# Kernel optimization log

Measured on AMD Instinct MI355X. Metric: run time of the kernel, lower is better.

## Reference

```python
import jax, jax.numpy as jnp
import numpy as np
import math

D_MODEL = 1024
FEAT = 16            # feature_dim
HEADS = 16
HEAD_DIM = D_MODEL // HEADS          # 64
EXP = 1 + FEAT + FEAT * FEAT         # 273, expanded (Taylor) feature dim
BATCH = 4
SEQ = 2048


def taylor_exp(x):
    """2nd-order Taylor feature map: [1, x/d^{1/4}, (x ox x)/(sqrt(2)*sqrt(d))]."""
    d = x.shape[-1]
    r2 = math.sqrt(2.0)
    rd = math.sqrt(d)
    rrd = math.sqrt(rd)
    x2 = (x[..., :, None] * x[..., None, :]).reshape(*x.shape[:-1], d * d) / r2
    return jnp.concatenate([jnp.ones_like(x[..., :1]), x / rrd, x2 / rd], axis=-1)


def setup_inputs() -> dict:
    key = jax.random.key(0)
    ks = jax.random.split(key, 9)
    s_in = 1.0 / math.sqrt(D_MODEL)
    inp = {
        "x": jax.random.normal(ks[0], (BATCH, SEQ, D_MODEL), dtype=jnp.float32),
        "kv_state": jnp.zeros((BATCH, HEADS, EXP, HEAD_DIM), dtype=jnp.float32),
        "k_state": jnp.zeros((BATCH, HEADS, EXP), dtype=jnp.float32),
        # Linear params stored as [in, out] (y = x @ W + b)
        "Wq": jax.random.normal(ks[1], (D_MODEL, FEAT * HEADS), dtype=jnp.float32) * s_in,
        "bq": jnp.zeros((FEAT * HEADS,), dtype=jnp.float32),
        "Wk": jax.random.normal(ks[2], (D_MODEL, FEAT * HEADS), dtype=jnp.float32) * s_in,
        "bk": jnp.zeros((FEAT * HEADS,), dtype=jnp.float32),
        "Wv": jax.random.normal(ks[3], (D_MODEL, HEAD_DIM * HEADS), dtype=jnp.float32) * s_in,
        "bv": jnp.zeros((HEAD_DIM * HEADS,), dtype=jnp.float32),
        "Wo": jax.random.normal(ks[4], (HEADS * HEAD_DIM, D_MODEL), dtype=jnp.float32) * s_in,
        "bo": jnp.zeros((D_MODEL,), dtype=jnp.float32),
    }
    return inp


def _forward(x, kv_state, k_state, Wq, bq, Wk, bk, Wv, bv, Wo, bo):
    b, l, _ = x.shape
    # projections -> b h l d
    q = (x @ Wq + bq).reshape(b, l, HEADS, FEAT).transpose(0, 2, 1, 3)
    k = (x @ Wk + bk).reshape(b, l, HEADS, FEAT).transpose(0, 2, 1, 3)
    v = (x @ Wv + bv).reshape(b, l, HEADS, HEAD_DIM).transpose(0, 2, 1, 3)
    q = taylor_exp(q)  # b h l EXP
    k = taylor_exp(k)  # b h l EXP

    # scan over time: carry (kv_state [b,h,EXP,hd], k_state [b,h,EXP])
    qs = jnp.moveaxis(q, 2, 0)  # l b h EXP
    ks = jnp.moveaxis(k, 2, 0)  # l b h EXP
    vs = jnp.moveaxis(v, 2, 0)  # l b h hd

    def step(carry, qkv_t):
        kv, kst = carry
        q_t, k_t, v_t = qkv_t
        kv = kv + k_t[..., :, None] * v_t[..., None, :]   # b h EXP hd
        kst = kst + k_t                                    # b h EXP
        num = jnp.einsum('bhd,bhdc->bhc', q_t, kv)
        den = jnp.einsum('bhd,bhd->bh', q_t, kst) + 1e-6
        return (kv, kst), num / den[..., None]

    (kv_f, kst_f), outs = jax.lax.scan(step, (kv_state, k_state), (qs, ks, vs))
    # outs: l b h hd -> b l (h hd)
    y = jnp.moveaxis(outs, 0, 1).reshape(b, l, HEADS * HEAD_DIM)
    y = y @ Wo + bo  # dropout is identity in eval mode
    return y, kv_f, kst_f


def reference(x, kv_state, k_state, Wq, bq, Wk, bk, Wv, bv, Wo, bo):
    return _forward(x, kv_state, k_state, Wq, bq, Wk, bk, Wv, bv, Wo, bo)
```

## Files before the change

### kernel.cpp

```cpp
#include <hip/hip_runtime.h>

typedef unsigned short u16;
typedef __attribute__((ext_vector_type(8))) short bf16x8;
typedef __attribute__((ext_vector_type(4))) float f32x4;

#define BATCH 4
#define SEQ   2048
#define DM    1024
#define HEADS 16
#define FEAT  16
#define HD    64
#define EXPD  273
#define EXPP  288
#define CHK   128
#define NC    16
#define BH    64
#define QKS   512
#define MROWS 8192
#define C2    0.17677669529663687f

__device__ __forceinline__ u16 f2b(float f) {
  union { float f; unsigned u; } v; v.f = f;
  unsigned u = v.u;
  return (u16)((u + 0x7fffu + ((u >> 16) & 1u)) >> 16);
}
__device__ __forceinline__ float b2f(u16 s) {
  union { unsigned u; float f; } v; v.u = ((unsigned)s) << 16; return v.f;
}

typedef const unsigned int __attribute__((address_space(1)))* gas1;
typedef unsigned int __attribute__((address_space(3)))* las3;
__device__ __forceinline__ void gl_lds16(const u16* g, u16* l) {
  __builtin_amdgcn_global_load_lds((gas1)(const void*)g, (las3)(void*)l, 16, 0, 0);
}

__global__ __launch_bounds__(256) void prep(const float* __restrict__ x, u16* __restrict__ xb,
                                            const float* __restrict__ Wq, const float* __restrict__ Wk,
                                            const float* __restrict__ Wv, const float* __restrict__ Wo,
                                            u16* __restrict__ wqkvT, u16* __restrict__ woT,
                                            const float* __restrict__ bq, const float* __restrict__ bk,
                                            const float* __restrict__ bv, float* __restrict__ bias_all) {
  __shared__ float tile[32][33];
  int id = blockIdx.x;
  if (id < 8192) {
    int i = id * 256 + threadIdx.x;
    float4 v = ((const float4*)x)[i];
    u16 r[4] = {f2b(v.x), f2b(v.y), f2b(v.z), f2b(v.w)};
    ((uint2*)xb)[i] = *(uint2*)r;
    return;
  }
  id -= 8192;
  if (id < 2560) {
    const float* src; u16* dst; int N, t;
    if (id < 256)       { src = Wq; dst = wqkvT;            N = 256;  t = id; }
    else if (id < 512)  { src = Wk; dst = wqkvT + 256 * DM; N = 256;  t = id - 256; }
    else if (id < 1536) { src = Wv; dst = wqkvT + 512 * DM; N = 1024; t = id - 512; }
    else                { src = Wo; dst = woT;              N = 1024; t = id - 1536; }
    int nt = N / 32;
    int n0 = (t % nt) * 32, k0 = (t / nt) * 32;
    int tx = threadIdx.x & 31, ty = threadIdx.x >> 5;
    for (int i = ty; i < 32; i += 8)
      tile[i][tx] = src[(size_t)(k0 + i) * N + n0 + tx];
    __syncthreads();
    for (int i = ty; i < 32; i += 8)
      dst[(size_t)(n0 + i) * DM + k0 + tx] = f2b(tile[tx][i]);
    return;
  }
  id -= 2560;
  int i = id * 256 + threadIdx.x;
  float v;
  if (i < 256) v = bq[i];
  else if (i < 512) v = bk[i - 256];
  else v = bv[i - 512];
  bias_all[i] = v;
}

__global__ __launch_bounds__(256) void gemmQKV(const u16* __restrict__ A, const u16* __restrict__ BT,
                                               const float* __restrict__ bias,
                                               float* __restrict__ qkw, u16* __restrict__ vbT) {
  __shared__ __align__(16) u16 As[128 * 32];
  __shared__ __align__(16) u16 Bs[128 * 32];
  const int tid = threadIdx.x;
  const int wave = tid >> 6, lane = tid & 63, qd = lane >> 4, ln = lane & 15;
  const int wr = (wave >> 1) * 64, wc = (wave & 1) * 64;
  const int m0 = blockIdx.y * 128, n0 = blockIdx.x * 128;
  const int K = DM;
  f32x4 acc[4][4];
#pragma unroll
  for (int i = 0; i < 4; i++)
#pragma unroll
    for (int j = 0; j < 4; j++) acc[i][j] = (f32x4){0.f, 0.f, 0.f, 0.f};
  const int sr = tid >> 2, sk = (tid & 3) * 8;
  const u16* gA0 = A + (size_t)(m0 + sr) * K + sk;
  const u16* gA1 = A + (size_t)(m0 + 64 + sr) * K + sk;
  const u16* gB0 = BT + (size_t)(n0 + sr) * K + sk;
  const u16* gB1 = BT + (size_t)(n0 + 64 + sr) * K + sk;
  u16* lA0 = &As[(size_t)(wave * 64) * 8];
  u16* lA1 = &As[(size_t)(256 + wave * 64) * 8];
  u16* lB0 = &Bs[(size_t)(wave * 64) * 8];
  u16* lB1 = &Bs[(size_t)(256 + wave * 64) * 8];
  for (int kk = 0; kk < K; kk += 32) {
    gl_lds16(gA0 + kk, lA0);
    gl_lds16(gA1 + kk, lA1);
    gl_lds16(gB0 + kk, lB0);
    gl_lds16(gB1 + kk, lB1);
    __syncthreads();
    bf16x8 af[4], bf[4];
#pragma unroll
    for (int t = 0; t < 4; t++) {
      af[t] = *(const bf16x8*)&As[(wr + t * 16 + ln) * 32 + qd * 8];
      bf[t] = *(const bf16x8*)&Bs[(wc + t * 16 + ln) * 32 + qd * 8];
    }
#pragma unroll
    for (int mt = 0; mt < 4; mt++)
#pragma unroll
      for (int nt = 0; nt < 4; nt++)
        acc[mt][nt] = __builtin_amdgcn_mfma_f32_16x16x32_bf16(af[mt], bf[nt], acc[mt][nt], 0, 0, 0);
    __syncthreads();
  }
  if (n0 < 512) {
#pragma unroll
    for (int nt = 0; nt < 4; nt++) {
      int col = n0 + wc + nt * 16 + ln;
      float bv = bias[col];
#pragma unroll
      for (int mt = 0; mt < 4; mt++)
#pragma unroll
        for (int r = 0; r < 4; r++) {
          int row = m0 + wr + mt * 16 + qd * 4 + r;
          qkw[(size_t)row * QKS + col] = acc[mt][nt][r] + bv;
        }
    }
  } else {
#pragma unroll
    for (int nt = 0; nt < 4; nt++) {
      int col = n0 + wc + nt * 16 + ln;
      float bv = bias[col];
      int vcol = col - 512;
#pragma unroll
      for (int mt = 0; mt < 4; mt++) {
        u16 pk[4];
#pragma unroll
        for (int r = 0; r < 4; r++) pk[r] = f2b(acc[mt][nt][r] + bv);
        int row0 = m0 + wr + mt * 16 + qd * 4;
        *(uint2*)&vbT[(size_t)vcol * MROWS + row0] = *(uint2*)pk;
      }
    }
  }
}

__global__ __launch_bounds__(256) void gemm128(const u16* __restrict__ A, const u16* __restrict__ BT,
                                               const float* __restrict__ bias, int M, int N, int K,
                                               float* __restrict__ outF) {
  __shared__ __align__(16) u16 As[128 * 32];
  __shared__ __align__(16) u16 Bs[128 * 32];
  const int tid = threadIdx.x;
  const int wave = tid >> 6, lane = tid & 63, qd = lane >> 4, ln = lane & 15;
  const int wr = (wave >> 1) * 64, wc = (wave & 1) * 64;
  const int m0 = blockIdx.y * 128, n0 = blockIdx.x * 128;
  f32x4 acc[4][4];
#pragma unroll
  for (int i = 0; i < 4; i++)
#pragma unroll
    for (int j = 0; j < 4; j++) acc[i][j] = (f32x4){0.f, 0.f, 0.f, 0.f};
  const int sr = tid >> 2, sk = (tid & 3) * 8;
  const u16* gA0 = A + (size_t)(m0 + sr) * K + sk;
  const u16* gA1 = A + (size_t)(m0 + 64 + sr) * K + sk;
  const u16* gB0 = BT + (size_t)(n0 + sr) * K + sk;
  const u16* gB1 = BT + (size_t)(n0 + 64 + sr) * K + sk;
  u16* lA0 = &As[(size_t)(wave * 64) * 8];
  u16* lA1 = &As[(size_t)(256 + wave * 64) * 8];
  u16* lB0 = &Bs[(size_t)(wave * 64) * 8];
  u16* lB1 = &Bs[(size_t)(256 + wave * 64) * 8];
  for (int kk = 0; kk < K; kk += 32) {
    gl_lds16(gA0 + kk, lA0);
    gl_lds16(gA1 + kk, lA1);
    gl_lds16(gB0 + kk, lB0);
    gl_lds16(gB1 + kk, lB1);
    __syncthreads();
    bf16x8 af[4], bf[4];
#pragma unroll
    for (int t = 0; t < 4; t++) {
      af[t] = *(const bf16x8*)&As[(wr + t * 16 + ln) * 32 + qd * 8];
      bf[t] = *(const bf16x8*)&Bs[(wc + t * 16 + ln) * 32 + qd * 8];
    }
#pragma unroll
    for (int mt = 0; mt < 4; mt++)
#pragma unroll
      for (int nt = 0; nt < 4; nt++)
        acc[mt][nt] = __builtin_amdgcn_mfma_f32_16x16x32_bf16(af[mt], bf[nt], acc[mt][nt], 0, 0, 0);
    __syncthreads();
  }
#pragma unroll
  for (int nt = 0; nt < 4; nt++) {
    int col = n0 + wc + nt * 16 + ln;
    float bv = bias[col];
#pragma unroll
    for (int mt = 0; mt < 4; mt++)
#pragma unroll
      for (int r = 0; r < 4; r++) {
        int row = m0 + wr + mt * 16 + qd * 4 + r;
        outF[(size_t)row * N + col] = acc[mt][nt][r] + bv;
      }
  }
}

template<int KT>
__device__ __forceinline__ void feat_row(const float* q16, int p, u16* dst) {
  u16 pk[16];
  if (KT == 0 && p == 0) {
    pk[0] = 0x3F80;
#pragma unroll
    for (int j = 1; j < 16; j++) pk[j] = f2b(0.5f * q16[j - 1]);
  } else if (KT == 0) {
    pk[0] = f2b(0.5f * q16[15]);
    float wm = C2 * q16[0];
#pragma unroll
    for (int j = 1; j < 16; j++) pk[j] = f2b(wm * q16[j - 1]);
  } else {
    constexpr int c = 2 * KT;
    float wm = C2 * (p ? q16[c]     : q16[c - 1]);
    float w0 = C2 * (p ? q16[c - 1] : q16[c - 2]);
    pk[0] = f2b(w0 * q16[15]);
#pragma unroll
    for (int j = 1; j < 16; j++) pk[j] = f2b(wm * q16[j - 1]);
    if (KT == 8 && p) {
#pragma unroll
      for (int j = 1; j < 16; j++) pk[j] = 0;
    }
  }
  *(uint4*)dst = *(uint4*)pk;
  *(uint4*)(dst + 8) = *(uint4*)(pk + 8);
}

template<int MTB>
__device__ __forceinline__ void kfeat(const float* k16, int p, int t2, u16 (*kfT)[16][136]) {
  u16 pk[16];
  if (MTB == 0) {
    if (p == 0) {
      pk[0] = 0x3F80;
#pragma unroll
      for (int j = 1; j < 16; j++) pk[j] = f2b(0.5f * k16[j - 1]);
    } else {
      float w0 = C2 * k16[0], wm = C2 * k16[1];
      pk[0] = f2b(w0 * k16[15]);
#pragma unroll
      for (int j = 1; j < 16; j++) pk[j] = f2b(wm * k16[j - 1]);
    }
  } else if (MTB == 1) {
    if (p == 0) {
      pk[0] = f2b(0.5f * k16[15]);
      float wm = C2 * k16[0];
#pragma unroll
      for (int j = 1; j < 16; j++) pk[j] = f2b(wm * k16[j - 1]);
    } else {
      float w0 = C2 * k16[1], wm = C2 * k16[2];
      pk[0] = f2b(w0 * k16[15]);
#pragma unroll
      for (int j = 1; j < 16; j++) pk[j] = f2b(wm * k16[j - 1]);
    }
  } else {
    float wm = C2 * (p ? k16[MTB + 1] : k16[MTB - 1]);
    float w0 = C2 * (p ? k16[MTB]     : k16[MTB - 2]);
    pk[0] = f2b(w0 * k16[15]);
#pragma unroll
    for (int j = 1; j < 16; j++) pk[j] = f2b(wm * k16[j - 1]);
  }
  int b = 2 * p + (MTB & 1);
#pragma unroll
  for (int el = 0; el < 16; el++) kfT[b][el][t2] = pk[el];
}

__global__ __launch_bounds__(256) void chunk_sums(const float* __restrict__ qkw, const u16* __restrict__ vbT,
                                                  u16* __restrict__ ckvT, float* __restrict__ ck) {
  __shared__ float kl[CHK][20];
  __shared__ __align__(16) u16 kfT[4][16][136];
  const int tid = threadIdx.x;
  const int bh = blockIdx.x / NC, c = blockIdx.x % NC;
  const int b = bh >> 4, h = bh & 15;
  const int wave = tid >> 6, lane = tid & 63, qd = lane >> 4, ln = lane & 15;
  const int t2 = tid >> 1, p = tid & 1;
  const size_t rowbase = (size_t)(b * SEQ + c * CHK);
  float k16[16];
  {
    const float* kp = &qkw[(rowbase + t2) * QKS + 256 + h * FEAT];
    float4 v0 = *(const float4*)kp, v1 = *(const float4*)(kp + 4);
    float4 v2 = *(const float4*)(kp + 8), v3 = *(const float4*)(kp + 12);
    k16[0] = v0.x; k16[1] = v0.y; k16[2] = v0.z; k16[3] = v0.w;
    k16[4] = v1.x; k16[5] = v1.y; k16[6] = v1.z; k16[7] = v1.w;
    k16[8] = v2.x; k16[9] = v2.y; k16[10] = v2.z; k16[11] = v2.w;
    k16[12] = v3.x; k16[13] = v3.y; k16[14] = v3.z; k16[15] = v3.w;
    float4 h0, h1;
    if (p == 0) { h0 = v0; h1 = v1; } else { h0 = v2; h1 = v3; }
    *(float4*)&kl[t2][p * 8] = h0;
    *(float4*)&kl[t2][p * 8 + 4] = h1;
  }
  uint4 bVv[4][4];
#pragma unroll
  for (int kk2 = 0; kk2 < 4; kk2++)
#pragma unroll
    for (int nt = 0; nt < 4; nt++)
      bVv[kk2][nt] = *(const uint4*)&vbT[(size_t)(h * HD + nt * 16 + ln) * MROWS +
                                         rowbase + kk2 * 32 + qd * 8];
  const size_t obase = (size_t)(bh * NC + c) * HD;
  auto mstore = [&](int mt, int bufw) {
    f32x4 acc[4];
#pragma unroll
    for (int nt = 0; nt < 4; nt++) acc[nt] = (f32x4){0.f, 0.f, 0.f, 0.f};
#pragma unroll
    for (int kk2 = 0; kk2 < 4; kk2++) {
      bf16x8 a = *(const bf16x8*)&kfT[bufw][ln][kk2 * 32 + qd * 8];
#pragma unroll
      for (int nt = 0; nt < 4; nt++) {
        bf16x8 bb = *(const bf16x8*)&bVv[kk2][nt];
        acc[nt] = __builtin_amdgcn_mfma_f32_16x16x32_bf16(a, bb, acc[nt], 0, 0, 0);
      }
    }
#pragma unroll
    for (int nt = 0; nt < 4; nt++) {
      u16 pk[4];
#pragma unroll
      for (int r = 0; r < 4; r++) pk[r] = f2b(acc[nt][r]);
      *(uint2*)&ckvT[(obase + nt * 16 + ln) * EXPP + mt * 16 + qd * 4] = *(uint2*)pk;
    }
  };
  __syncthreads();
  kfeat<0>(k16, p, t2, kfT); kfeat<1>(k16, p, t2, kfT);
  __syncthreads();
  mstore(wave, wave);
  __syncthreads();
  kfeat<4>(k16, p, t2, kfT); kfeat<5>(k16, p, t2, kfT);
  __syncthreads();
  mstore(4 + wave, wave);
  __syncthreads();
  kfeat<8>(k16, p, t2, kfT); kfeat<9>(k16, p, t2, kfT);
  __syncthreads();
  mstore(8 + wave, wave);
  __syncthreads();
  kfeat<12>(k16, p, t2, kfT); kfeat<13>(k16, p, t2, kfT);
  __syncthreads();
  mstore(12 + wave, wave);
  __syncthreads();
  {
    u16 pk[16];
    if (p == 0) {
      float w0 = C2 * k16[14], wm = C2 * k16[15];
      pk[0] = f2b(w0 * k16[15]);
#pragma unroll
      for (int j = 1; j < 16; j++) pk[j] = f2b(wm * k16[j - 1]);
    } else {
      pk[0] = f2b(C2 * k16[15] * k16[15]);
#pragma unroll
      for (int j = 1; j < 16; j++) pk[j] = 0;
    }
#pragma unroll
    for (int el = 0; el < 16; el++) kfT[p][el][t2] = pk[el];
  }
  __syncthreads();
  if (wave < 2) mstore(16 + wave, wave);
  for (int e = tid; e < EXPP; e += 256) {
    float s = 0.f;
    if (e == 0) s = (float)CHK;
    else if (e < 17) { float t = 0.f; for (int tt = 0; tt < CHK; tt++) t += kl[tt][e - 1]; s = 0.5f * t; }
    else if (e < EXPD) {
      int u = e - 17, i0 = u >> 4, j0 = u & 15; float t = 0.f;
      for (int tt = 0; tt < CHK; tt++) t += kl[tt][i0] * kl[tt][j0];
      s = C2 * t;
    }
    ck[(size_t)(bh * NC + c) * EXPP + e] = s;
  }
}

__global__ __launch_bounds__(256) void kv_prefix(u16* __restrict__ ckvT, const float* __restrict__ kv0,
                                                 float* __restrict__ out_kv,
                                                 float* __restrict__ ck, const float* __restrict__ k0,
                                                 float* __restrict__ out_k) {
  const int tid = threadIdx.x;
  const int bh = blockIdx.x / 10, eg = blockIdx.x % 10;
  if (eg == 9) {
    for (int e = tid; e < EXPP; e += 256) {
      float S = (e < EXPD) ? k0[(size_t)bh * EXPD + e] : 0.f;
      for (int c = 0; c < NC; c++) {
        size_t idx = ((size_t)bh * NC + c) * EXPP + e;
        float v = ck[idx];
        ck[idx] = S;
        S += v;
      }
      if (e < EXPD) out_k[(size_t)bh * EXPD + e] = S;
    }
    return;
  }
  const int hd = tid >> 2;
  const int e0 = eg * 32 + (tid & 3) * 8;
  float S[8];
#pragma unroll
  for (int j = 0; j < 8; j++) {
    int e = e0 + j;
    S[j] = (e < EXPD) ? kv0[((size_t)bh * EXPD + e) * HD + hd] : 0.f;
  }
  u16* base = ckvT + ((size_t)bh * NC * HD + hd) * EXPP + e0;
  const size_t cstride = (size_t)HD * EXPP;
  uint4 v0 = *(const uint4*)base;
  uint4 v1 = *(const uint4*)(base + cstride);
  for (int c = 0; c < NC; c++) {
    uint4 vn = v1;
    if (c + 2 < NC) vn = *(const uint4*)(base + (size_t)(c + 2) * cstride);
    union { uint4 q; u16 s[8]; } pk;
#pragma unroll
    for (int j = 0; j < 8; j++) pk.s[j] = f2b(S[j]);
    *(uint4*)(base + (size_t)c * cstride) = pk.q;
    union { uint4 q; u16 s[8]; } vv; vv.q = v0;
#pragma unroll
    for (int j = 0; j < 8; j++) S[j] += b2f(vv.s[j]);
    v0 = v1; v1 = vn;
  }
#pragma unroll
  for (int j = 0; j < 8; j++) {
    int e = e0 + j;
    if (e < EXPD) out_kv[((size_t)bh * EXPD + e) * HD + hd] = S[j];
  }
}

__global__ __launch_bounds__(256) void out_chunk(const float* __restrict__ qkw, const u16* __restrict__ vbT,
                                                 const u16* __restrict__ ckvT, const float* __restrict__ ck,
                                                 u16* __restrict__ ob) {
  __shared__ __align__(16) u16 pool[18432];
  __shared__ float kstl[EXPP];
  __shared__ float denl[CHK];
  u16 (*qlb)[40] = (u16(*)[40])pool;
  u16 (*klb)[32] = (u16(*)[32])(pool + 5120);
  u16 (*qfs)[40] = (u16(*)[40])(pool + 9216);
  u16 (*alB)[72] = (u16(*)[72])pool;
  u16 (*alA)[72] = (u16(*)[72])(pool + 9216);
  const int tid = threadIdx.x;
  const int bh = blockIdx.x / NC, c = blockIdx.x % NC;
  const int b = bh >> 4, h = bh & 15;
  const int wave = tid >> 6, lane = tid & 63, qd = lane >> 4, ln = lane & 15;
  const int t2 = tid >> 1, p = tid & 1;
  const size_t rowbase = (size_t)(b * SEQ + c * CHK);
  float q16[16];
  {
    const float* qp = &qkw[(rowbase + t2) * QKS + h * FEAT];
    float4 v0 = *(const float4*)qp, v1 = *(const float4*)(qp + 4);
    float4 v2 = *(const float4*)(qp + 8), v3 = *(const float4*)(qp + 12);
    q16[0] = v0.x; q16[1] = v0.y; q16[2] = v0.z; q16[3] = v0.w;
    q16[4] = v1.x; q16[5] = v1.y; q16[6] = v1.z; q16[7] = v1.w;
    q16[8] = v2.x; q16[9] = v2.y; q16[10] = v2.z; q16[11] = v2.w;
    q16[12] = v3.x; q16[13] = v3.y; q16[14] = v3.z; q16[15] = v3.w;
    u16 qb[8];
#pragma unroll
    for (int j = 0; j < 8; j++) qb[j] = f2b(q16[p * 8 + j]);
    *(uint4*)&qlb[t2][p * 8] = *(uint4*)qb;
    *(uint4*)&qlb[t2][16 + p * 8] = (uint4){0u, 0u, 0u, 0u};
    const float* kp = &qkw[(rowbase + t2) * QKS + 256 + h * FEAT + p * 8];
    float4 k0v = *(const float4*)kp, k1v = *(const float4*)(kp + 4);
    u16 kb[8] = {f2b(k0v.x), f2b(k0v.y), f2b(k0v.z), f2b(k0v.w),
                 f2b(k1v.x), f2b(k1v.y), f2b(k1v.z), f2b(k1v.w)};
    *(uint4*)&klb[t2][p * 8] = *(uint4*)kb;
    *(uint4*)&klb[t2][16 + p * 8] = (uint4){0u, 0u, 0u, 0u};
  }
  const size_t cbase = (size_t)(bh * NC + c);
  for (int e = tid; e < EXPP; e += 256) kstl[e] = ck[cbase * EXPP + e];
  const u16* sptr = ckvT + (cbase * HD + wave * 16 + ln) * EXPP + qd * 8;
  uint4 bSv[9];
#pragma unroll
  for (int kt = 0; kt < 9; kt++) bSv[kt] = *(const uint4*)(sptr + kt * 32);
  uint4 bVv[4];
#pragma unroll
  for (int kk2 = 0; kk2 < 4; kk2++)
    bVv[kk2] = *(const uint4*)&vbT[(size_t)(h * HD + wave * 16 + ln) * MROWS +
                                   rowbase + kk2 * 32 + qd * 8];
  feat_row<0>(q16, p, &qfs[t2][p * 16]);
  __syncthreads();
  f32x4 accO[8];
#pragma unroll
  for (int nt = 0; nt < 8; nt++) accO[nt] = (f32x4){0.f, 0.f, 0.f, 0.f};
#define KSTEP(KT)                                                                          \
  {                                                                                        \
    bf16x8 aS = *(const bf16x8*)&bSv[(KT)];                                                \
    _Pragma("unroll")                                                                      \
    for (int nt = 0; nt < 8; nt++) {                                                       \
      bf16x8 bQ = *(const bf16x8*)&qfs[nt * 16 + ln][qd * 8];                              \
      accO[nt] = __builtin_amdgcn_mfma_f32_16x16x32_bf16(aS, bQ, accO[nt], 0, 0, 0);       \
    }                                                                                      \
    __syncthreads();                                                                       \
    if ((KT) < 8) {                                                                        \
      feat_row<(KT) + 1>(q16, p, &qfs[t2][p * 16]);                                        \
      __syncthreads();                                                                     \
    }                                                                                      \
  }
  KSTEP(0) KSTEP(1) KSTEP(2) KSTEP(3) KSTEP(4) KSTEP(5) KSTEP(6) KSTEP(7) KSTEP(8)
#undef KSTEP
  {
    f32x4 accU[8];
    bf16x8 aK = *(const bf16x8*)&klb[wave * 16 + ln][qd * 8];
#pragma unroll
    for (int nt = 0; nt < 8; nt++) {
      bf16x8 bQ = *(const bf16x8*)&qlb[nt * 16 + ln][qd * 8];
      accU[nt] = __builtin_amdgcn_mfma_f32_16x16x32_bf16(aK, bQ, (f32x4){0.f, 0.f, 0.f, 0.f}, 0, 0, 0);
    }
#pragma unroll
    for (int nt = 0; nt < 8; nt++) {
      int t = nt * 16 + ln, sb = wave * 16 + qd * 4;
      u16 pk[4];
#pragma unroll
      for (int r = 0; r < 4; r++) {
        float u = accU[nt][r];
        float sc = 1.f + 0.25f * u + 0.03125f * u * u;
        pk[r] = (sb + r <= t) ? f2b(sc) : (u16)0;
      }
      *(uint2*)&alA[t][sb] = *(uint2*)pk;
    }
  }
  {
    f32x4 accU[8];
    bf16x8 aK = *(const bf16x8*)&klb[(wave + 4) * 16 + ln][qd * 8];
#pragma unroll
    for (int nt = 0; nt < 8; nt++) {
      bf16x8 bQ = *(const bf16x8*)&qlb[nt * 16 + ln][qd * 8];
      accU[nt] = __builtin_amdgcn_mfma_f32_16x16x32_bf16(aK, bQ, (f32x4){0.f, 0.f, 0.f, 0.f}, 0, 0, 0);
    }
    __syncthreads();
#pragma unroll
    for (int nt = 0; nt < 8; nt++) {
      int t = nt * 16 + ln, sbl = wave * 16 + qd * 4;
      u16 pk[4];
#pragma unroll
      for (int r = 0; r < 4; r++) {
        float u = accU[nt][r];
        float sc = 1.f + 0.25f * u + 0.03125f * u * u;
        pk[r] = (64 + sbl + r <= t) ? f2b(sc) : (u16)0;
      }
      *(uint2*)&alB[t][sbl] = *(uint2*)pk;
    }
  }
  __syncthreads();
#pragma unroll
  for (int kk2 = 0; kk2 < 4; kk2++) {
    bf16x8 aV = *(const bf16x8*)&bVv[kk2];
#pragma unroll
    for (int nt = 0; nt < 8; nt++) {
      bf16x8 bA = (kk2 < 2) ? *(const bf16x8*)&alA[nt * 16 + ln][kk2 * 32 + qd * 8]
                            : *(const bf16x8*)&alB[nt * 16 + ln][(kk2 - 2) * 32 + qd * 8];
      accO[nt] = __builtin_amdgcn_mfma_f32_16x16x32_bf16(aV, bA, accO[nt], 0, 0, 0);
    }
  }
  {
    float s = 0.f;
#pragma unroll
    for (int i2 = 0; i2 < 8; i2++) {
      int i = p * 8 + i2;
      float inner = 0.f;
#pragma unroll
      for (int j = 0; j < 16; j++) inner += q16[j] * kstl[17 + i * 16 + j];
      s += q16[i] * inner;
    }
    s *= C2;
    float s1 = 0.f;
#pragma unroll
    for (int j2 = 0; j2 < 8; j2++) s1 += q16[p * 8 + j2] * kstl[1 + p * 8 + j2];
    s += 0.5f * s1;
    if (p == 0) s += kstl[0] + 1e-6f;
    const u16* arow = p ? &alB[t2][0] : &alA[t2][0];
    float da = 0.f;
#pragma unroll
    for (int sb = 0; sb < 8; sb++) {
      union { uint4 q; u16 hh[8]; } uu;
      uu.q = *(const uint4*)(arow + sb * 8);
#pragma unroll
      for (int j = 0; j < 8; j++) da += b2f(uu.hh[j]);
    }
    s += da;
    s += __shfl_xor(s, 1);
    if (p == 0) denl[t2] = s;
  }
  __syncthreads();
#pragma unroll
  for (int nt = 0; nt < 8; nt++) {
    int t = nt * 16 + ln;
    float dn = denl[t];
    u16 pk[4];
#pragma unroll
    for (int r = 0; r < 4; r++) pk[r] = f2b(accO[nt][r] / dn);
    *(uint2*)&ob[(rowbase + t) * DM + h * HD + wave * 16 + qd * 4] = *(uint2*)pk;
  }
}

extern "C" void kernel_launch(void* const* d_in, const int* in_sizes, int n_in,
                              void* d_out, int out_size, void* d_ws, size_t ws_size,
                              hipStream_t stream) {
  (void)in_sizes; (void)n_in; (void)out_size;
  const float* x   = (const float*)d_in[0];
  const float* kv0 = (const float*)d_in[1];
  const float* k0  = (const float*)d_in[2];
  const float* bq  = (const float*)d_in[4];
  const float* bk  = (const float*)d_in[6];
  const float* bv  = (const float*)d_in[8];
  const float* bo  = (const float*)d_in[10];
  float* out = (float*)d_out;
  char* ws = (char*)d_ws;
  size_t off = 0;
  auto take = [&](size_t bytes) { char* p = ws + off; off += (bytes + 255) & ~(size_t)255; return p; };
  u16*   xb     = (u16*)  take((size_t)BATCH * SEQ * DM * 2);
  u16*   wqkvT  = (u16*)  take((size_t)1536 * DM * 2);
  u16*   woT    = (u16*)  take((size_t)DM * DM * 2);
  float* bias_a = (float*)take((size_t)1536 * 4);
  float* qkw    = (float*)take((size_t)BATCH * SEQ * QKS * 4);
  u16*   vbT    = (u16*)  take((size_t)BATCH * SEQ * DM * 2);
  u16*   ckvT   = (u16*)  take((size_t)BH * NC * EXPP * HD * 2);
  float* ck     = (float*)take((size_t)BH * NC * EXPP * 4);
  u16*   ob     = (u16*)  take((size_t)BATCH * SEQ * DM * 2);
  if (off > ws_size) return;

  float* out_kv = out + (size_t)BATCH * SEQ * DM;
  float* out_k  = out_kv + (size_t)BH * EXPD * HD;

  prep<<<8192 + 2560 + 6, 256, 0, stream>>>(x, xb,
      (const float*)d_in[3], (const float*)d_in[5], (const float*)d_in[7], (const float*)d_in[9],
      wqkvT, woT, bq, bk, bv, bias_a);

  gemmQKV<<<dim3(12, 64), 256, 0, stream>>>(xb, wqkvT, bias_a, qkw, vbT);

  chunk_sums<<<BH * NC, 256, 0, stream>>>(qkw, vbT, ckvT, ck);
  kv_prefix<<<BH * 10, 256, 0, stream>>>(ckvT, kv0, out_kv, ck, k0, out_k);
  out_chunk<<<BH * NC, 256, 0, stream>>>(qkw, vbT, ckvT, ck, ob);

  gemm128<<<dim3(8, 64), 256, 0, stream>>>(ob, woT, bo, MROWS, DM, DM, out);
}
```

Before: 292.8 us.

## Double-buffer and widen GEMM tiles to 128x256 with swizzled LDS

```diff
diff --git a/kernel.cpp b/kernel.cpp
--- a/kernel.cpp
+++ b/kernel.cpp
@@ -75,52 +75,68 @@
   bias_all[i] = v;
 }
 
-__global__ __launch_bounds__(256) void gemmQKV(const u16* __restrict__ A, const u16* __restrict__ BT,
-                                               const float* __restrict__ bias,
-                                               float* __restrict__ qkw, u16* __restrict__ vbT) {
-  __shared__ __align__(16) u16 As[128 * 32];
-  __shared__ __align__(16) u16 Bs[128 * 32];
+__global__ __launch_bounds__(256, 2) void gemmQKV(const u16* __restrict__ A, const u16* __restrict__ BT,
+                                                  const float* __restrict__ bias,
+                                                  float* __restrict__ qkw, u16* __restrict__ vbT) {
+  __shared__ __align__(16) u16 As[2][128 * 32];
+  __shared__ __align__(16) u16 Bs[2][256 * 32];
   const int tid = threadIdx.x;
   const int wave = tid >> 6, lane = tid & 63, qd = lane >> 4, ln = lane & 15;
-  const int wr = (wave >> 1) * 64, wc = (wave & 1) * 64;
-  const int m0 = blockIdx.y * 128, n0 = blockIdx.x * 128;
+  const int wr = (wave >> 1) * 64, wc = (wave & 1) * 128;
+  const int m0 = blockIdx.y * 128, n0 = blockIdx.x * 256;
   const int K = DM;
-  f32x4 acc[4][4];
+  f32x4 acc[4][8];
 #pragma unroll
   for (int i = 0; i < 4; i++)
 #pragma unroll
-    for (int j = 0; j < 4; j++) acc[i][j] = (f32x4){0.f, 0.f, 0.f, 0.f};
-  const int sr = tid >> 2, sk = (tid & 3) * 8;
-  const u16* gA0 = A + (size_t)(m0 + sr) * K + sk;
-  const u16* gA1 = A + (size_t)(m0 + 64 + sr) * K + sk;
-  const u16* gB0 = BT + (size_t)(n0 + sr) * K + sk;
-  const u16* gB1 = BT + (size_t)(n0 + 64 + sr) * K + sk;
-  u16* lA0 = &As[(size_t)(wave * 64) * 8];
-  u16* lA1 = &As[(size_t)(256 + wave * 64) * 8];
-  u16* lB0 = &Bs[(size_t)(wave * 64) * 8];
-  u16* lB1 = &Bs[(size_t)(256 + wave * 64) * 8];
-  for (int kk = 0; kk < K; kk += 32) {
-    gl_lds16(gA0 + kk, lA0);
-    gl_lds16(gA1 + kk, lA1);
-    gl_lds16(gB0 + kk, lB0);
-    gl_lds16(gB1 + kk, lB1);
-    __syncthreads();
-    bf16x8 af[4], bf[4];
-#pragma unroll
-    for (int t = 0; t < 4; t++) {
-      af[t] = *(const bf16x8*)&As[(wr + t * 16 + ln) * 32 + qd * 8];
-      bf[t] = *(const bf16x8*)&Bs[(wc + t * 16 + ln) * 32 + qd * 8];
-    }
+    for (int j = 0; j < 8; j++) acc[i][j] = (f32x4){0.f, 0.f, 0.f, 0.f};
+  const int sr = tid >> 2;
+  const int scs = (((tid & 3) ^ ((sr >> 1) & 3))) * 8;
+  const u16* gA0 = A + (size_t)(m0 + sr) * K + scs;
+  const u16* gA1 = gA0 + (size_t)64 * K;
+  const u16* gB0 = BT + (size_t)(n0 + sr) * K + scs;
+  auto stage = [&](int buf, int kk) {
+    gl_lds16(gA0 + kk, &As[buf][wave * 512]);
+    gl_lds16(gA1 + kk, &As[buf][2048 + wave * 512]);
+    gl_lds16(gB0 + kk,                    &Bs[buf][wave * 512]);
+    gl_lds16(gB0 + (size_t)64 * K + kk,   &Bs[buf][2048 + wave * 512]);
+    gl_lds16(gB0 + (size_t)128 * K + kk,  &Bs[buf][4096 + wave * 512]);
+    gl_lds16(gB0 + (size_t)192 * K + kk,  &Bs[buf][6144 + wave * 512]);
+  };
+  const int swz = ((ln >> 1) & 3) << 3;
+  auto compute = [&](int buf) {
+    bf16x8 af[4], bf[8];
+#pragma unroll
+    for (int t = 0; t < 4; t++)
+      af[t] = *(const bf16x8*)&As[buf][(wr + t * 16 + ln) * 32 + ((qd * 8) ^ swz)];
+#pragma unroll
+    for (int u = 0; u < 8; u++)
+      bf[u] = *(const bf16x8*)&Bs[buf][(wc + u * 16 + ln) * 32 + ((qd * 8) ^ swz)];
 #pragma unroll
     for (int mt = 0; mt < 4; mt++)
 #pragma unroll
-      for (int nt = 0; nt < 4; nt++)
+      for (int nt = 0; nt < 8; nt++)
         acc[mt][nt] = __builtin_amdgcn_mfma_f32_16x16x32_bf16(af[mt], bf[nt], acc[mt][nt], 0, 0, 0);
-    __syncthreads();
-  }
+  };
+  stage(0, 0);
+  int buf = 0;
+  for (int kk = 32; kk < K; kk += 32) {
+    stage(buf ^ 1, kk);
+    asm volatile("s_waitcnt vmcnt(6)" ::: "memory");
+    __builtin_amdgcn_s_barrier();
+    asm volatile("" ::: "memory");
+    compute(buf);
+    asm volatile("" ::: "memory");
+    __builtin_amdgcn_s_barrier();
+    buf ^= 1;
+  }
+  asm volatile("s_waitcnt vmcnt(0)" ::: "memory");
+  __builtin_amdgcn_s_barrier();
+  asm volatile("" ::: "memory");
+  compute(buf);
   if (n0 < 512) {
 #pragma unroll
-    for (int nt = 0; nt < 4; nt++) {
+    for (int nt = 0; nt < 8; nt++) {
       int col = n0 + wc + nt * 16 + ln;
       float bv = bias[col];
 #pragma unroll
@@ -133,7 +149,7 @@
     }
   } else {
 #pragma unroll
-    for (int nt = 0; nt < 4; nt++) {
+    for (int nt = 0; nt < 8; nt++) {
       int col = n0 + wc + nt * 16 + ln;
       float bv = bias[col];
       int vcol = col - 512;
@@ -149,50 +165,66 @@
   }
 }
 
-__global__ __launch_bounds__(256) void gemm128(const u16* __restrict__ A, const u16* __restrict__ BT,
-                                               const float* __restrict__ bias, int M, int N, int K,
-                                               float* __restrict__ outF) {
-  __shared__ __align__(16) u16 As[128 * 32];
-  __shared__ __align__(16) u16 Bs[128 * 32];
+__global__ __launch_bounds__(256, 2) void gemm128(const u16* __restrict__ A, const u16* __restrict__ BT,
+                                                  const float* __restrict__ bias, int M, int N, int K,
+                                                  float* __restrict__ outF) {
+  __shared__ __align__(16) u16 As[2][128 * 32];
+  __shared__ __align__(16) u16 Bs[2][256 * 32];
   const int tid = threadIdx.x;
   const int wave = tid >> 6, lane = tid & 63, qd = lane >> 4, ln = lane & 15;
-  const int wr = (wave >> 1) * 64, wc = (wave & 1) * 64;
-  const int m0 = blockIdx.y * 128, n0 = blockIdx.x * 128;
-  f32x4 acc[4][4];
+  const int wr = (wave >> 1) * 64, wc = (wave & 1) * 128;
+  const int m0 = blockIdx.y * 128, n0 = blockIdx.x * 256;
+  f32x4 acc[4][8];
 #pragma unroll
   for (int i = 0; i < 4; i++)
 #pragma unroll
-    for (int j = 0; j < 4; j++) acc[i][j] = (f32x4){0.f, 0.f, 0.f, 0.f};
-  const int sr = tid >> 2, sk = (tid & 3) * 8;
-  const u16* gA0 = A + (size_t)(m0 + sr) * K + sk;
-  const u16* gA1 = A + (size_t)(m0 + 64 + sr) * K + sk;
-  const u16* gB0 = BT + (size_t)(n0 + sr) * K + sk;
-  const u16* gB1 = BT + (size_t)(n0 + 64 + sr) * K + sk;
-  u16* lA0 = &As[(size_t)(wave * 64) * 8];
-  u16* lA1 = &As[(size_t)(256 + wave * 64) * 8];
-  u16* lB0 = &Bs[(size_t)(wave * 64) * 8];
-  u16* lB1 = &Bs[(size_t)(256 + wave * 64) * 8];
-  for (int kk = 0; kk < K; kk += 32) {
-    gl_lds16(gA0 + kk, lA0);
-    gl_lds16(gA1 + kk, lA1);
-    gl_lds16(gB0 + kk, lB0);
-    gl_lds16(gB1 + kk, lB1);
-    __syncthreads();
-    bf16x8 af[4], bf[4];
-#pragma unroll
-    for (int t = 0; t < 4; t++) {
-      af[t] = *(const bf16x8*)&As[(wr + t * 16 + ln) * 32 + qd * 8];
-      bf[t] = *(const bf16x8*)&Bs[(wc + t * 16 + ln) * 32 + qd * 8];
-    }
+    for (int j = 0; j < 8; j++) acc[i][j] = (f32x4){0.f, 0.f, 0.f, 0.f};
+  const int sr = tid >> 2;
+  const int scs = (((tid & 3) ^ ((sr >> 1) & 3))) * 8;
+  const u16* gA0 = A + (size_t)(m0 + sr) * K + scs;
+  const u16* gA1 = gA0 + (size_t)64 * K;
+  const u16* gB0 = BT + (size_t)(n0 + sr) * K + scs;
+  auto stage = [&](int buf, int kk) {
+    gl_lds16(gA0 + kk, &As[buf][wave * 512]);
+    gl_lds16(gA1 + kk, &As[buf][2048 + wave * 512]);
+    gl_lds16(gB0 + kk,                    &Bs[buf][wave * 512]);
+    gl_lds16(gB0 + (size_t)64 * K + kk,   &Bs[buf][2048 + wave * 512]);
+    gl_lds16(gB0 + (size_t)128 * K + kk,  &Bs[buf][4096 + wave * 512]);
+    gl_lds16(gB0 + (size_t)192 * K + kk,  &Bs[buf][6144 + wave * 512]);
+  };
+  const int swz = ((ln >> 1) & 3) << 3;
+  auto compute = [&](int buf) {
+    bf16x8 af[4], bf[8];
+#pragma unroll
+    for (int t = 0; t < 4; t++)
+      af[t] = *(const bf16x8*)&As[buf][(wr + t * 16 + ln) * 32 + ((qd * 8) ^ swz)];
+#pragma unroll
+    for (int u = 0; u < 8; u++)
+      bf[u] = *(const bf16x8*)&Bs[buf][(wc + u * 16 + ln) * 32 + ((qd * 8) ^ swz)];
 #pragma unroll
     for (int mt = 0; mt < 4; mt++)
 #pragma unroll
-      for (int nt = 0; nt < 4; nt++)
+      for (int nt = 0; nt < 8; nt++)
         acc[mt][nt] = __builtin_amdgcn_mfma_f32_16x16x32_bf16(af[mt], bf[nt], acc[mt][nt], 0, 0, 0);
-    __syncthreads();
-  }
-#pragma unroll
-  for (int nt = 0; nt < 4; nt++) {
+  };
+  stage(0, 0);
+  int buf = 0;
+  for (int kk = 32; kk < K; kk += 32) {
+    stage(buf ^ 1, kk);
+    asm volatile("s_waitcnt vmcnt(6)" ::: "memory");
+    __builtin_amdgcn_s_barrier();
+    asm volatile("" ::: "memory");
+    compute(buf);
+    asm volatile("" ::: "memory");
+    __builtin_amdgcn_s_barrier();
+    buf ^= 1;
+  }
+  asm volatile("s_waitcnt vmcnt(0)" ::: "memory");
+  __builtin_amdgcn_s_barrier();
+  asm volatile("" ::: "memory");
+  compute(buf);
+#pragma unroll
+  for (int nt = 0; nt < 8; nt++) {
     int col = n0 + wc + nt * 16 + ln;
     float bv = bias[col];
 #pragma unroll
@@ -619,11 +651,11 @@
       (const float*)d_in[3], (const float*)d_in[5], (const float*)d_in[7], (const float*)d_in[9],
       wqkvT, woT, bq, bk, bv, bias_a);
 
-  gemmQKV<<<dim3(12, 64), 256, 0, stream>>>(xb, wqkvT, bias_a, qkw, vbT);
+  gemmQKV<<<dim3(6, 64), 256, 0, stream>>>(xb, wqkvT, bias_a, qkw, vbT);
 
   chunk_sums<<<BH * NC, 256, 0, stream>>>(qkw, vbT, ckvT, ck);
   kv_prefix<<<BH * 10, 256, 0, stream>>>(ckvT, kv0, out_kv, ck, k0, out_k);
   out_chunk<<<BH * NC, 256, 0, stream>>>(qkw, vbT, ckvT, ck, ob);
 
-  gemm128<<<dim3(8, 64), 256, 0, stream>>>(ob, woT, bo, MROWS, DM, DM, out);
-}
+  gemm128<<<dim3(4, 64), 256, 0, stream>>>(ob, woT, bo, MROWS, DM, DM, out);
+}
```

Measured after the change: 294.0 us. About the same (+0.4%).
